# Optimization experiments

Measured on AMD Instinct MI355X. Metric: run time of the kernel, lower is better.

## Reference

```python
import jax, jax.numpy as jnp
import numpy as np

TSZ_SCALE = 1000000.0
N = 256                     # map size (hard-coded in the module)
NBINS = 64                  # len(ell)
PS = 5 * 60 / 256           # arcmin per pixel
RAD_PER_PIX = PS * np.pi / 180.0
EPS = 1e-12


def _bin_segment_ids():
    """Reproduce the module's radial bin assignment (np.digitize on |L|2D)."""
    lx = 2 * np.pi * np.fft.fftfreq(N, d=RAD_PER_PIX)
    mg = np.meshgrid(lx, lx)
    L2D = np.sqrt(mg[0] ** 2 + mg[1] ** 2)
    ell_min = 2 * np.pi / (N * RAD_PER_PIX)
    ell_max = np.max(L2D)
    bins = np.linspace(ell_min, ell_max, NBINS + 1)
    bin_indices = np.digitize(L2D.flatten(), bins) - 1  # in [-1, NBINS]
    # shift by +1 so out-of-range low values (-1) land in segment 0;
    # high out-of-range values land in segment NBINS+1; valid bins are 1..NBINS
    seg = np.clip(bin_indices + 1, 0, NBINS + 1).astype(np.int32)
    return seg


def setup_inputs() -> dict:
    key = jax.random.key(0)
    pred = jax.random.normal(key, (1024, N, N), dtype=jnp.float32)
    ell = jnp.arange(1, NBINS + 1, dtype=jnp.float32) * 200.0
    w = ell ** 3
    weighting = w / w.mean()
    mean_cl = jnp.full((NBINS,), 1e-6, dtype=jnp.float32)
    seg_ids = jnp.asarray(_bin_segment_ids())  # [65536] int32
    return {"pred": pred, "mean_cl": mean_cl, "weighting": weighting,
            "seg_ids": seg_ids}


def reference(pred, mean_cl, weighting, seg_ids):
    B = pred.shape[0]
    pred_unscaled = pred / TSZ_SCALE
    pred_fft = jnp.fft.fft2(pred_unscaled)                       # [B,256,256] complex
    ps2d = (jnp.abs(pred_fft) ** 2) * (RAD_PER_PIX ** 2) / (N * N)
    flat = ps2d.reshape(B, -1)                                   # [B, 65536]
    # segment mean over pixels == dense matmul with row-normalized binning matrix B
    sums = jax.ops.segment_sum(flat.T, seg_ids, num_segments=NBINS + 2).T  # [B, NBINS+2]
    counts = jax.ops.segment_sum(jnp.ones((N * N,), dtype=flat.dtype), seg_ids,
                                 num_segments=NBINS + 2)
    inv_counts = jnp.where(counts > 0, 1.0 / counts, 0.0)
    ps1d = sums[:, 1:NBINS + 1] * inv_counts[1:NBINS + 1][None, :]  # [B, NBINS]
    diff = jnp.log(ps1d + EPS) - jnp.log(mean_cl + EPS)[None, :]
    return jnp.mean(weighting[None, :] * diff ** 2)
```

## Files before the change

### kernel.cpp

```cpp
#include <hip/hip_runtime.h>
#include <hip/hip_fp16.h>
#include <math.h>

#define NSEG 66
typedef unsigned uv2 __attribute__((ext_vector_type(2)));
typedef unsigned h2u;

__device__ __forceinline__ int brev6(int l) {
    return ((l&1)<<5)|((l&2)<<3)|((l&4)<<1)|((l&8)>>1)|((l&16)>>3)|((l&32)>>5);
}
__device__ __forceinline__ h2u f2h(float a, float b) {
    __half2 h = __floats2half2_rn(a, b); return *reinterpret_cast<unsigned*>(&h);
}
__device__ __forceinline__ h2u shflu(h2u x, int src) {
    return __float_as_uint(__shfl(__uint_as_float(x), src));
}

__device__ __forceinline__ h2u pkh_fma(h2u a, h2u b, h2u c) {
    h2u d; asm("v_pk_fma_f16 %0, %1, %2, %3" : "=v"(d) : "v"(a), "v"(b), "v"(c));
    return d;
}
__device__ __forceinline__ h2u pkh_mul(h2u a, h2u b) {
    h2u d; asm("v_pk_mul_f16 %0, %1, %2" : "=v"(d) : "v"(a), "v"(b));
    return d;
}
__device__ __forceinline__ h2u pkh_add(h2u a, h2u b) {
    h2u d; asm("v_pk_add_f16 %0, %1, %2" : "=v"(d) : "v"(a), "v"(b));
    return d;
}
__device__ __forceinline__ h2u pkh_sub(h2u a, h2u b) {
    h2u d; asm("v_pk_add_f16 %0, %1, %2 neg_lo:[0,1] neg_hi:[0,1]" : "=v"(d) : "v"(a), "v"(b));
    return d;
}
__device__ __forceinline__ h2u pkh_addmi(h2u a, h2u b) {
    h2u d; asm("v_pk_add_f16 %0, %1, %2 op_sel:[0,1] op_sel_hi:[1,0] neg_hi:[0,1]"
               : "=v"(d) : "v"(a), "v"(b));
    return d;
}
__device__ __forceinline__ h2u pkh_addpi(h2u a, h2u b) {
    h2u d; asm("v_pk_add_f16 %0, %1, %2 op_sel:[0,1] op_sel_hi:[1,0] neg_lo:[0,1]"
               : "=v"(d) : "v"(a), "v"(b));
    return d;
}
__device__ __forceinline__ h2u cmulh(h2u z, h2u ta, h2u tb) {
    h2u p, r;
    asm("v_pk_mul_f16 %0, %1, %2 op_sel:[0,0] op_sel_hi:[1,0]" : "=v"(p) : "v"(z), "v"(ta));
    asm("v_pk_fma_f16 %0, %1, %2, %3 op_sel:[1,0,0] op_sel_hi:[0,1,1]"
        : "=v"(r) : "v"(z), "v"(tb), "v"(p));
    return r;
}
__device__ __forceinline__ h2u pkh_mul_sw0(h2u a, h2u b) {
    h2u d; asm("v_pk_mul_f16 %0, %1, %2 op_sel:[1,0] op_sel_hi:[0,1]" : "=v"(d) : "v"(a), "v"(b));
    return d;
}
__device__ __forceinline__ h2u pkh_fma_sw0(h2u a, h2u b, h2u c) {
    h2u d; asm("v_pk_fma_f16 %0, %1, %2, %3 op_sel:[1,0,0] op_sel_hi:[0,1,1]"
               : "=v"(d) : "v"(a), "v"(b), "v"(c));
    return d;
}
__device__ __forceinline__ float pow2h(h2u X) {
    float p; const float zf = 0.f;
    asm("v_fma_mix_f32 %0, %2, %2, %1 op_sel:[0,0,0] op_sel_hi:[1,1,0]" : "=v"(p) : "v"(zf), "v"(X));
    asm("v_fma_mix_f32 %0, %1, %1, %0 op_sel:[1,1,0] op_sel_hi:[1,1,0]" : "+v"(p) : "v"(X));
    return p;
}
__device__ __forceinline__ unsigned bperm(unsigned hi, unsigned lo, unsigned sel) {
#if __has_builtin(__builtin_amdgcn_perm)
    return __builtin_amdgcn_perm(hi, lo, sel);
#else
    unsigned long long v = ((unsigned long long)hi << 32) | lo;
    unsigned r = 0;
    for (int b = 0; b < 4; ++b) r |= ((unsigned)(v >> (8*((sel>>(8*b))&7))) & 0xFF) << (8*b);
    return r;
#endif
}

#define C_PP 0x38003800u
#define C_PM 0xB8003800u

struct XTH {
    h2u ta32, tb32, sg32;
    h2u ta16, tb16, sg16;
    h2u ta8,  tb8,  sg8;
    h2u ta4,  tb4,  sg4;
    h2u ta2,  tb2,  sg2;
    h2u sg1;
    h2u wa1, wb1, wa2, wb2, wa3, wb3;
    int pl;
};

__device__ __forceinline__ h2u bflyh_pl32(h2u z, h2u sg, h2u ta, h2u tb) {
#if __has_builtin(__builtin_amdgcn_permlane32_swap)
    uv2 r = __builtin_amdgcn_permlane32_swap(z, z, false, false);
    h2u u = pkh_fma(r[1], sg, r[0]);
#else
    h2u c = shflu(z, 0); (void)c;
    h2u u = pkh_fma(z, sg, __float_as_uint(__shfl_xor(__uint_as_float(z), 32)));
#endif
    return cmulh(u, ta, tb);
}
__device__ __forceinline__ h2u bflyh_pl16(h2u z, h2u sg, h2u ta, h2u tb) {
#if __has_builtin(__builtin_amdgcn_permlane16_swap)
    uv2 r = __builtin_amdgcn_permlane16_swap(z, z, false, false);
    h2u u = pkh_fma(r[1], sg, r[0]);
#else
    h2u u = pkh_fma(z, sg, __float_as_uint(__shfl_xor(__uint_as_float(z), 16)));
#endif
    return cmulh(u, ta, tb);
}
template<int CTRL>
__device__ __forceinline__ h2u dppx(h2u x) {
#if __has_builtin(__builtin_amdgcn_update_dpp)
    return (h2u)__builtin_amdgcn_update_dpp((int)x, (int)x, CTRL, 0xF, 0xF, false);
#else
    const int d = (CTRL == 0x128) ? 8 : (CTRL == 0x4E ? 2 : 1);
    return __float_as_uint(__shfl_xor(__uint_as_float(x), d));
#endif
}
template<int CTRL>
__device__ __forceinline__ h2u bflyh_dpp(h2u z, h2u sg, h2u ta, h2u tb) {
    return cmulh(pkh_fma(z, sg, dppx<CTRL>(z)), ta, tb);
}
__device__ __forceinline__ h2u bflyh1(h2u z, h2u sg) {
    return pkh_fma(z, sg, dppx<0xB1>(z));
}
__device__ __forceinline__ h2u bflyh_ds4(h2u z, h2u sg, h2u ta, h2u tb) {
    h2u c = (h2u)__builtin_amdgcn_ds_swizzle((int)z, 0x101F);
    return cmulh(pkh_fma(z, sg, c), ta, tb);
}

__device__ __forceinline__ float dpp_scan64(float x, int L) {
#if __has_builtin(__builtin_amdgcn_update_dpp)
    #define UPD(ctrl, rmask) __int_as_float(__builtin_amdgcn_update_dpp( \
        0, __float_as_int(x), ctrl, rmask, 0xF, false))
    x += UPD(0x111, 0xF);
    x += UPD(0x112, 0xF);
    x += UPD(0x114, 0xF);
    x += UPD(0x118, 0xF);
    x += UPD(0x142, 0xA);
    x += UPD(0x143, 0xC);
    #undef UPD
    return x;
#else
    #pragma unroll
    for (int off = 1; off < 64; off <<= 1) {
        const float yv = __shfl_up(x, off);
        if (L >= off) x += yv;
    }
    return x;
#endif
}

__device__ __forceinline__ void fft64x4h(h2u z[4], const XTH& T) {
    #pragma unroll
    for (int a = 0; a < 4; ++a) {
        z[a] = bflyh_pl32(z[a], T.sg32, T.ta32, T.tb32);
        z[a] = bflyh_pl16(z[a], T.sg16, T.ta16, T.tb16);
        z[a] = bflyh_dpp<0x128>(z[a], T.sg8, T.ta8, T.tb8);
        z[a] = bflyh_ds4(z[a], T.sg4, T.ta4, T.tb4);
        z[a] = bflyh_dpp<0x4E>(z[a], T.sg2, T.ta2, T.tb2);
        z[a] = bflyh1(z[a], T.sg1);
    }
}
__device__ __forceinline__ void twdft4h(const h2u z[4], const XTH& T, h2u X[4]) {
    h2u g0 = z[0];
    h2u g1 = cmulh(z[1], T.wa1, T.wb1);
    h2u g2 = cmulh(z[2], T.wa2, T.wb2);
    h2u g3 = cmulh(z[3], T.wa3, T.wb3);
    h2u b0 = pkh_add(g0, g2), b1 = pkh_sub(g0, g2);
    h2u b2 = pkh_add(g1, g3), b3 = pkh_sub(g1, g3);
    X[0] = pkh_add(b0, b2);
    X[2] = pkh_sub(b0, b2);
    X[1] = pkh_addmi(b1, b3);
    X[3] = pkh_addpi(b1, b3);
}

__global__ __launch_bounds__(896, 7)
void k_fused(const float* __restrict__ pred, const int4* __restrict__ tbl,
             const int* __restrict__ cnt, const float* __restrict__ mean_cl,
             const float* __restrict__ weighting, float* __restrict__ out,
             float cscale, float invB64) {
    __shared__ __align__(16) unsigned short tile[128 * 256];
    __shared__ __align__(16) float pbuf[14][256];
    const int tid = threadIdx.x, w = tid >> 6, L = tid & 63;
    const int rL = brev6(L);
    const float PI2 = 6.283185307179586f;

    XTH T;
    {
        auto stw = [&](int d, h2u& ta, h2u& tb, h2u& sg) {
            const float s = (L & d) ? -1.f : 1.f;
            const int e = (L & d) ? (L & (d-1)) * (32/d) : 0;
            float ss, cc; __sincosf(-PI2 * (float)e / 64.f, &ss, &cc);
            ta = f2h(cc, ss); tb = f2h(-ss, ss); sg = f2h(s, s);
        };
        stw(32, T.ta32, T.tb32, T.sg32);
        stw(16, T.ta16, T.tb16, T.sg16);
        stw( 8, T.ta8,  T.tb8,  T.sg8);
        stw( 4, T.ta4,  T.tb4,  T.sg4);
        stw( 2, T.ta2,  T.tb2,  T.sg2);
        const float s1 = (L & 1) ? -1.f : 1.f;
        T.sg1 = f2h(s1, s1);
        float sg, cg;
        __sincosf(-PI2 * (float)rL / 256.f, &sg, &cg);
        const float w2x = cg*cg - sg*sg, w2y = 2.f*cg*sg;
        const float w3x = w2x*cg - w2y*sg, w3y = w2x*sg + w2y*cg;
        T.wa1 = f2h(cg, sg);   T.wb1 = f2h(-sg, sg);
        T.wa2 = f2h(w2x, w2y); T.wb2 = f2h(-w2y, w2y);
        T.wa3 = f2h(w3x, w3y); T.wb3 = f2h(-w3y, w3y);
        T.pl = brev6((64 - rL) & 63);
    }

    const float* base = pred + (size_t)blockIdx.x * 65536;
    const int sw = rL & 28;
    #pragma unroll 2
    for (int p = w; p < 128; p += 14) {
        const int y = 2 * p;
        const float4 ra = *(const float4*)(base + (size_t)y*256 + 4*L);
        const float4 rb = *(const float4*)(base + (size_t)(y+1)*256 + 4*L);
        h2u z[4] = { f2h(ra.x, rb.x), f2h(ra.y, rb.y), f2h(ra.z, rb.z), f2h(ra.w, rb.w) };
        fft64x4h(z, T);
        h2u X[4]; twdft4h(z, T, X);
        h2u q0 = shflu(X[3], T.pl);
        h2u q1 = shflu(X[2], T.pl);
        if (L == 0) { q0 = X[0]; q1 = X[3]; }
        const int yi = y ^ sw;
        const h2u F = pkh_fma(q0, C_PM, pkh_mul(X[0], C_PP));
        const h2u G = pkh_fma_sw0(q0, C_PP, pkh_mul_sw0(X[0], C_PM));
        if (L == 0) {
            const unsigned tmp = bperm(G, F, 0x00000501u);
            const unsigned e   = bperm(X[2], tmp, 0x07010500u);
            *(unsigned*)&tile[y] = e;
        } else {
            const unsigned e = bperm(G, F, 0x07050301u);
            *(unsigned*)&tile[rL*256 + yi] = e;
        }
        {
            const h2u F2 = pkh_fma(q1, C_PM, pkh_mul(X[1], C_PP));
            const h2u G2 = pkh_fma_sw0(q1, C_PP, pkh_mul_sw0(X[1], C_PM));
            const unsigned e = bperm(G2, F2, 0x07050301u);
            *(unsigned*)&tile[(64+rL)*256 + yi] = e;
        }
    }
    __syncthreads();

    float acc = 0.f;
    float* pb = pbuf[w];
    auto binpass = [&](float p0, float p1, float p2, float p3, int4 tb) -> float {
        pb[rL] = p0; pb[rL+64] = p1; pb[rL+128] = p2; pb[rL+192] = p3;
        const float4 pv = ((const float4*)pb)[L];
        const float s0 = pv.x, s1 = s0+pv.y, s2 = s1+pv.z, s3 = s2+pv.w;
        const float x = dpp_scan64(s3, L);
        const float ex = x - s3;
        ((float4*)pb)[L] = make_float4(ex+s0, ex+s1, ex+s2, ex+s3);
        float gy = pb[tb.y & 255], gx = pb[tb.x & 255];
        float gw = pb[tb.w & 255], gz = pb[tb.z & 255];
        gy = (tb.y < 0) ? 0.f : gy;  gx = (tb.x < 0) ? 0.f : gx;
        gw = (tb.w < 0) ? 0.f : gw;  gz = (tb.z < 0) ? 0.f : gz;
        return gy - gx + gw - gz;
    };
    #pragma unroll 2
    for (int kx = w; kx <= 127; kx += 14) {
        const int cs = kx & 28;
        const uint2 uu = *(const uint2*)&tile[kx*256 + ((4*L) ^ cs)];
        h2u z[4] = { bperm(0u, uu.x, 0x01040004u), bperm(0u, uu.x, 0x03040204u),
                     bperm(0u, uu.y, 0x01040004u), bperm(0u, uu.y, 0x03040204u) };
        fft64x4h(z, T);
        h2u X[4]; twdft4h(z, T, X);
        if (kx == 0) {
            h2u Xp0 = shflu(X[3], T.pl), Xp1 = shflu(X[2], T.pl);
            h2u Xp2 = shflu(X[1], T.pl), Xp3 = shflu(X[0], T.pl);
            if (L == 0) { Xp0 = X[0]; Xp1 = X[3]; Xp2 = X[2]; Xp3 = X[1]; }
            const float a0 = pow2h(pkh_fma(Xp0, C_PM, pkh_mul(X[0], C_PP)));
            const float a1 = pow2h(pkh_fma(Xp1, C_PM, pkh_mul(X[1], C_PP)));
            const float a2 = pow2h(pkh_fma(Xp2, C_PM, pkh_mul(X[2], C_PP)));
            const float a3 = pow2h(pkh_fma(Xp3, C_PM, pkh_mul(X[3], C_PP)));
            const float b0 = pow2h(pkh_fma_sw0(Xp0, C_PP, pkh_mul_sw0(X[0], C_PM)));
            const float b1 = pow2h(pkh_fma_sw0(Xp1, C_PP, pkh_mul_sw0(X[1], C_PM)));
            const float b2 = pow2h(pkh_fma_sw0(Xp2, C_PP, pkh_mul_sw0(X[2], C_PM)));
            const float b3 = pow2h(pkh_fma_sw0(Xp3, C_PP, pkh_mul_sw0(X[3], C_PM)));
            const int4 tbA = tbl[0*64 + L];
            const int4 tbB = tbl[128*64 + L];
            acc += binpass(a0, a1, a2, a3, tbA);
            acc += binpass(b0, b1, b2, b3, tbB);
        } else {
            const int4 tb = tbl[kx*64 + L];
            const float p0 = pow2h(X[0]), p1 = pow2h(X[1]);
            const float p2 = pow2h(X[2]), p3 = pow2h(X[3]);
            acc = fmaf(2.f, binpass(p0, p1, p2, p3, tb), acc);
        }
    }
    __syncthreads();

    float* bins = (float*)tile;
    bins[w*64 + L] = acc;
    __syncthreads();
    if (tid < 64) {
        float tot = 0.f;
        #pragma unroll
        for (int ww = 0; ww < 14; ++ww) tot += bins[ww*64 + tid];
        const int c = cnt[tid + 1];
        const float inv = (c > 0) ? 1.0f / (float)c : 0.0f;
        const float v = tot * cscale * inv;
        const float d = logf(v + 1e-12f) - logf(mean_cl[tid] + 1e-12f);
        float l = weighting[tid] * d * d;
        #pragma unroll
        for (int o = 32; o; o >>= 1) l += __shfl_down(l, o);
        if (tid == 0) atomicAdd(out, l * invB64);
    }
}

__global__ __launch_bounds__(256) void k_prep(const int* __restrict__ seg,
                                              int4* __restrict__ tbl,
                                              int* __restrict__ cnt) {
    __shared__ int lo1[NSEG], hi1[NSEG], lo2[NSEG], hi2[NSEG], lc[NSEG];
    const int kx = blockIdx.x, ky = threadIdx.x;
    if (ky < NSEG) { lo1[ky] = 300; hi1[ky] = -1; lo2[ky] = 300; hi2[ky] = -1; lc[ky] = 0; }
    __syncthreads();
    const int s = seg[kx * 256 + ky];
    atomicAdd(&lc[s], 1);
    if (kx <= 128) {
        if (ky <= 128) { atomicMin(&lo1[s], ky); atomicMax(&hi1[s], ky); }
        else           { atomicMin(&lo2[s], ky); atomicMax(&hi2[s], ky); }
    }
    __syncthreads();
    if (ky < NSEG && lc[ky] > 0) atomicAdd(&cnt[ky], lc[ky]);
    if (kx <= 128 && ky >= 1 && ky <= 64) {
        int4 t;
        if (hi1[ky] < 0) { t.x = -1; t.y = -1; }
        else             { t.x = lo1[ky] - 1; t.y = hi1[ky]; }
        if (hi2[ky] < 0) { t.z = -1; t.w = -1; }
        else             { t.z = lo2[ky] - 1; t.w = hi2[ky]; }
        tbl[kx * 64 + (ky - 1)] = t;
    }
}

extern "C" void kernel_launch(void* const* d_in, const int* in_sizes, int n_in,
                              void* d_out, int out_size, void* d_ws, size_t ws_size,
                              hipStream_t stream) {
    const float* pred      = (const float*)d_in[0];
    const float* mean_cl   = (const float*)d_in[1];
    const float* weighting = (const float*)d_in[2];
    const int*   seg       = (const int*)d_in[3];
    float* out = (float*)d_out;

    const int B = in_sizes[0] / 65536;

    int*  cnt = (int*)d_ws;
    int4* tbl = (int4*)((char*)d_ws + 256);

    const double rad = (5.0 * 60.0 / 256.0) * M_PI / 180.0;
    const float cscale = (float)(rad * rad / (65536.0 * 1e12));
    const float invB64 = (float)(1.0 / ((double)B * 64.0));

    hipMemsetAsync(d_out, 0, sizeof(float), stream);
    hipMemsetAsync(cnt, 0, NSEG * sizeof(int), stream);
    k_prep<<<256, 256, 0, stream>>>(seg, tbl, cnt);
    k_fused<<<B, 896, 0, stream>>>(pred, tbl, cnt, mean_cl, weighting,
                                   out, cscale, invB64);
}
```

Baseline: 131.8 us.

## Widen FFT tile to packed half2 pairs and use 1024-thread blocks

Changes the shared-memory transpose tile from 16-bit entries to 32-bit packed half2 entries, so row-pass results are stored as uint2 and column-pass reads are a single uint4 with no byte-permute unpacking. Raises the block to 16 waves with a fixed 8-row-pair assignment per wave and pads each prefix buffer with a zero sentinel at index 256. The bin table now points empty or out-of-range entries at that sentinel, which removes the per-lookup masking and selects. The tile doubles to 128 KB of LDS, which limits blocks per CU and may lower occupancy.

```diff
diff --git a/kernel.cpp b/kernel.cpp
--- a/kernel.cpp
+++ b/kernel.cpp
@@ -94,8 +94,8 @@
     uv2 r = __builtin_amdgcn_permlane32_swap(z, z, false, false);
     h2u u = pkh_fma(r[1], sg, r[0]);
 #else
-    h2u c = shflu(z, 0); (void)c;
-    h2u u = pkh_fma(z, sg, __float_as_uint(__shfl_xor(__uint_as_float(z), 32)));
+    h2u c = __float_as_uint(__shfl_xor(__uint_as_float(z), 32));
+    h2u u = pkh_fma(z, sg, c);
 #endif
     return cmulh(u, ta, tb);
 }
@@ -104,7 +104,8 @@
     uv2 r = __builtin_amdgcn_permlane16_swap(z, z, false, false);
     h2u u = pkh_fma(r[1], sg, r[0]);
 #else
-    h2u u = pkh_fma(z, sg, __float_as_uint(__shfl_xor(__uint_as_float(z), 16)));
+    h2u c = __float_as_uint(__shfl_xor(__uint_as_float(z), 16));
+    h2u u = pkh_fma(z, sg, c);
 #endif
     return cmulh(u, ta, tb);
 }
@@ -175,13 +176,13 @@
     X[3] = pkh_addpi(b1, b3);
 }
 
-__global__ __launch_bounds__(896, 7)
+__global__ __launch_bounds__(1024)
 void k_fused(const float* __restrict__ pred, const int4* __restrict__ tbl,
              const int* __restrict__ cnt, const float* __restrict__ mean_cl,
              const float* __restrict__ weighting, float* __restrict__ out,
              float cscale, float invB64) {
-    __shared__ __align__(16) unsigned short tile[128 * 256];
-    __shared__ __align__(16) float pbuf[14][256];
+    __shared__ __align__(16) unsigned tile[128 * 256];
+    __shared__ __align__(16) float pbuf[16][260];
     const int tid = threadIdx.x, w = tid >> 6, L = tid & 63;
     const int rL = brev6(L);
     const float PI2 = 6.283185307179586f;
@@ -213,9 +214,9 @@
 
     const float* base = pred + (size_t)blockIdx.x * 65536;
     const int sw = rL & 28;
-    #pragma unroll 2
-    for (int p = w; p < 128; p += 14) {
-        const int y = 2 * p;
+    #pragma unroll 4
+    for (int t = 0; t < 8; ++t) {
+        const int y = 16*w + 2*t;
         const float4 ra = *(const float4*)(base + (size_t)y*256 + 4*L);
         const float4 rb = *(const float4*)(base + (size_t)(y+1)*256 + 4*L);
         h2u z[4] = { f2h(ra.x, rb.x), f2h(ra.y, rb.y), f2h(ra.z, rb.z), f2h(ra.w, rb.w) };
@@ -225,27 +226,30 @@
         h2u q1 = shflu(X[2], T.pl);
         if (L == 0) { q0 = X[0]; q1 = X[3]; }
         const int yi = y ^ sw;
-        const h2u F = pkh_fma(q0, C_PM, pkh_mul(X[0], C_PP));
-        const h2u G = pkh_fma_sw0(q0, C_PP, pkh_mul_sw0(X[0], C_PM));
-        if (L == 0) {
-            const unsigned tmp = bperm(G, F, 0x00000501u);
-            const unsigned e   = bperm(X[2], tmp, 0x07010500u);
-            *(unsigned*)&tile[y] = e;
-        } else {
-            const unsigned e = bperm(G, F, 0x07050301u);
-            *(unsigned*)&tile[rL*256 + yi] = e;
+        {
+            const h2u F = pkh_fma(q0, C_PM, pkh_mul(X[0], C_PP));
+            const h2u G = pkh_fma_sw0(q0, C_PP, pkh_mul_sw0(X[0], C_PM));
+            uint2 pk;
+            if (L == 0) {
+                pk.x = bperm(X[2], F, 0x05040100u);
+                pk.y = bperm(X[2], G, 0x07060100u);
+            } else {
+                pk.x = F; pk.y = G;
+            }
+            *(uint2*)&tile[rL*256 + yi] = pk;
         }
         {
-            const h2u F2 = pkh_fma(q1, C_PM, pkh_mul(X[1], C_PP));
-            const h2u G2 = pkh_fma_sw0(q1, C_PP, pkh_mul_sw0(X[1], C_PM));
-            const unsigned e = bperm(G2, F2, 0x07050301u);
-            *(unsigned*)&tile[(64+rL)*256 + yi] = e;
+            const h2u F = pkh_fma(q1, C_PM, pkh_mul(X[1], C_PP));
+            const h2u G = pkh_fma_sw0(q1, C_PP, pkh_mul_sw0(X[1], C_PM));
+            uint2 pk; pk.x = F; pk.y = G;
+            *(uint2*)&tile[(64+rL)*256 + yi] = pk;
         }
     }
     __syncthreads();
 
     float acc = 0.f;
     float* pb = pbuf[w];
+    if (L == 0) pb[256] = 0.f;
     auto binpass = [&](float p0, float p1, float p2, float p3, int4 tb) -> float {
         pb[rL] = p0; pb[rL+64] = p1; pb[rL+128] = p2; pb[rL+192] = p3;
         const float4 pv = ((const float4*)pb)[L];
@@ -253,18 +257,13 @@
         const float x = dpp_scan64(s3, L);
         const float ex = x - s3;
         ((float4*)pb)[L] = make_float4(ex+s0, ex+s1, ex+s2, ex+s3);
-        float gy = pb[tb.y & 255], gx = pb[tb.x & 255];
-        float gw = pb[tb.w & 255], gz = pb[tb.z & 255];
-        gy = (tb.y < 0) ? 0.f : gy;  gx = (tb.x < 0) ? 0.f : gx;
-        gw = (tb.w < 0) ? 0.f : gw;  gz = (tb.z < 0) ? 0.f : gz;
-        return gy - gx + gw - gz;
+        return pb[tb.y] - pb[tb.x] + pb[tb.w] - pb[tb.z];
     };
     #pragma unroll 2
-    for (int kx = w; kx <= 127; kx += 14) {
+    for (int kx = w; kx <= 127; kx += 16) {
         const int cs = kx & 28;
-        const uint2 uu = *(const uint2*)&tile[kx*256 + ((4*L) ^ cs)];
-        h2u z[4] = { bperm(0u, uu.x, 0x01040004u), bperm(0u, uu.x, 0x03040204u),
-                     bperm(0u, uu.y, 0x01040004u), bperm(0u, uu.y, 0x03040204u) };
+        const uint4 uu = *(const uint4*)&tile[kx*256 + ((4*L) ^ cs)];
+        h2u z[4] = { uu.x, uu.y, uu.z, uu.w };
         fft64x4h(z, T);
         h2u X[4]; twdft4h(z, T, X);
         if (kx == 0) {
@@ -279,10 +278,8 @@
             const float b1 = pow2h(pkh_fma_sw0(Xp1, C_PP, pkh_mul_sw0(X[1], C_PM)));
             const float b2 = pow2h(pkh_fma_sw0(Xp2, C_PP, pkh_mul_sw0(X[2], C_PM)));
             const float b3 = pow2h(pkh_fma_sw0(Xp3, C_PP, pkh_mul_sw0(X[3], C_PM)));
-            const int4 tbA = tbl[0*64 + L];
-            const int4 tbB = tbl[128*64 + L];
-            acc += binpass(a0, a1, a2, a3, tbA);
-            acc += binpass(b0, b1, b2, b3, tbB);
+            acc += binpass(a0, a1, a2, a3, tbl[0*64 + L]);
+            acc += binpass(b0, b1, b2, b3, tbl[128*64 + L]);
         } else {
             const int4 tb = tbl[kx*64 + L];
             const float p0 = pow2h(X[0]), p1 = pow2h(X[1]);
@@ -298,7 +295,7 @@
     if (tid < 64) {
         float tot = 0.f;
         #pragma unroll
-        for (int ww = 0; ww < 14; ++ww) tot += bins[ww*64 + tid];
+        for (int ww = 0; ww < 16; ++ww) tot += bins[ww*64 + tid];
         const int c = cnt[tid + 1];
         const float inv = (c > 0) ? 1.0f / (float)c : 0.0f;
         const float v = tot * cscale * inv;
@@ -327,9 +324,9 @@
     if (ky < NSEG && lc[ky] > 0) atomicAdd(&cnt[ky], lc[ky]);
     if (kx <= 128 && ky >= 1 && ky <= 64) {
         int4 t;
-        if (hi1[ky] < 0) { t.x = -1; t.y = -1; }
-        else             { t.x = lo1[ky] - 1; t.y = hi1[ky]; }
-        if (hi2[ky] < 0) { t.z = -1; t.w = -1; }
+        if (hi1[ky] < 0) { t.x = 256; t.y = 256; }
+        else             { t.x = (lo1[ky] > 0) ? lo1[ky] - 1 : 256; t.y = hi1[ky]; }
+        if (hi2[ky] < 0) { t.z = 256; t.w = 256; }
         else             { t.z = lo2[ky] - 1; t.w = hi2[ky]; }
         tbl[kx * 64 + (ky - 1)] = t;
     }
@@ -356,6 +353,6 @@
     hipMemsetAsync(d_out, 0, sizeof(float), stream);
     hipMemsetAsync(cnt, 0, NSEG * sizeof(int), stream);
     k_prep<<<256, 256, 0, stream>>>(seg, tbl, cnt);
-    k_fused<<<B, 896, 0, stream>>>(pred, tbl, cnt, mean_cl, weighting,
-                                   out, cscale, invB64);
-}
+    k_fused<<<B, 1024, 0, stream>>>(pred, tbl, cnt, mean_cl, weighting,
+                                    out, cscale, invB64);
+}
```

Measured after the change: 115.2 us. -12.6%, faster.
